# Kernel optimization log

Hardware: AMD Instinct MI355X
Metric: run time of the kernel (lower is better)

The kernel has to match this reference:

```python
import jax, jax.numpy as jnp
import numpy as np

B, D, L = 16384, 1024, 4

def setup_inputs() -> dict:
    key = jax.random.key(0)
    k1, k2 = jax.random.split(key)
    inputs = jax.random.normal(k1, (B, D), dtype=jnp.float32)
    # xavier_uniform for (D, 1): bound = sqrt(6/(D+1))
    bound = float(np.sqrt(6.0 / (D + 1)))
    weights = jax.random.uniform(k2, (L, D), dtype=jnp.float32, minval=-bound, maxval=bound)
    biases = jnp.zeros((L, D), dtype=jnp.float32)
    return {"inputs": inputs, "weights": weights, "biases": biases}

def reference(inputs, weights, biases):
    # inputs: [B, D]; weights/biases: [L, D]
    x0 = inputs

    def step(x, wb):
        w, b = wb
        xw = jnp.einsum("bd,d->b", x, w)          # x^T w  -> [B]
        x_next = x0 * xw[:, None] + b[None, :] + x  # outer product + bias + residual
        return x_next, None

    out, _ = jax.lax.scan(step, x0, (weights, biases))
    return out
```

## Files before the change

### kernel.cpp

```cpp
#include <hip/hip_runtime.h>


#define NB 16384
#define ROWS_PER_WAVE 4
#define NWAVES 4
#define ROWS_PER_BLOCK (ROWS_PER_WAVE * NWAVES)
#define NBLOCKS (NB / ROWS_PER_BLOCK)

#define DOT4(a, b) ((a).x*(b).x + (a).y*(b).y + (a).z*(b).z + (a).w*(b).w)

__global__ __launch_bounds__(256, 4) void crossnet_fused(
    const float* __restrict__ X,
    const float* __restrict__ W,
    const float* __restrict__ Bias,
    float* __restrict__ Out) {
  __shared__ float4 lds_u4[256];
  __shared__ float lds_s[NWAVES][3];

  const int t = threadIdx.x;
  const int wave = t >> 6;
  const int lane = t & 63;

  const float4* W4 = (const float4*)W;
  const float4* B4 = (const float4*)Bias;

  float4 b0 = B4[t];
  float4 b1 = B4[256 + t];
  float4 b2 = B4[512 + t];
  float4 b3 = B4[768 + t];
  float4 w1t = W4[256 + t];
  float4 w2t = W4[512 + t];
  float4 w3t = W4[768 + t];

  float4 u = b0;
  float s1p = DOT4(u, w1t);
  u.x += b1.x; u.y += b1.y; u.z += b1.z; u.w += b1.w;
  float s2p = DOT4(u, w2t);
  u.x += b2.x; u.y += b2.y; u.z += b2.z; u.w += b2.w;
  float s3p = DOT4(u, w3t);
  u.x += b3.x; u.y += b3.y; u.z += b3.z; u.w += b3.w;
  lds_u4[t] = u;

#pragma unroll
  for (int off = 32; off >= 1; off >>= 1) {
    s1p += __shfl_xor(s1p, off, 64);
    s2p += __shfl_xor(s2p, off, 64);
    s3p += __shfl_xor(s3p, off, 64);
  }
  if (lane == 0) {
    lds_s[wave][0] = s1p;
    lds_s[wave][1] = s2p;
    lds_s[wave][2] = s3p;
  }

  float4 w[4][4];
#pragma unroll
  for (int l = 0; l < 4; ++l)
#pragma unroll
    for (int k = 0; k < 4; ++k)
      w[l][k] = W4[l * 256 + lane + 64 * k];

  __syncthreads();

  const float s1 = lds_s[0][0] + lds_s[1][0] + lds_s[2][0] + lds_s[3][0];
  const float s2 = lds_s[0][1] + lds_s[1][1] + lds_s[2][1] + lds_s[3][1];
  const float s3 = lds_s[0][2] + lds_s[1][2] + lds_s[2][2] + lds_s[3][2];

  float4 u4r[4];
#pragma unroll
  for (int k = 0; k < 4; ++k) u4r[k] = lds_u4[lane + 64 * k];

  const int row0 = blockIdx.x * ROWS_PER_BLOCK + wave * ROWS_PER_WAVE;
#pragma unroll
  for (int r = 0; r < ROWS_PER_WAVE; ++r) {
    const int row = row0 + r;
    const float4* Xr = (const float4*)X + (size_t)row * 256;
    float4* Or = (float4*)Out + (size_t)row * 256;

    float4 x[4];
#pragma unroll
    for (int k = 0; k < 4; ++k) x[k] = Xr[lane + 64 * k];

    float p0 = 0.f, p1 = 0.f, p2 = 0.f, p3 = 0.f;
#pragma unroll
    for (int k = 0; k < 4; ++k) {
      p0 += DOT4(x[k], w[0][k]);
      p1 += DOT4(x[k], w[1][k]);
      p2 += DOT4(x[k], w[2][k]);
      p3 += DOT4(x[k], w[3][k]);
    }

#pragma unroll
    for (int off = 32; off >= 1; off >>= 1) {
      p0 += __shfl_xor(p0, off, 64);
      p1 += __shfl_xor(p1, off, 64);
      p2 += __shfl_xor(p2, off, 64);
      p3 += __shfl_xor(p3, off, 64);
    }

    float c = 1.0f;
    c = c * (p0 + 1.0f);
    c = c * (p1 + 1.0f) + s1;
    c = c * (p2 + 1.0f) + s2;
    c = c * (p3 + 1.0f) + s3;

#pragma unroll
    for (int k = 0; k < 4; ++k) {
      float4 o;
      o.x = c * x[k].x + u4r[k].x;
      o.y = c * x[k].y + u4r[k].y;
      o.z = c * x[k].z + u4r[k].z;
      o.w = c * x[k].w + u4r[k].w;
      Or[lane + 64 * k] = o;
    }
  }
}

extern "C" void kernel_launch(void* const* d_in, const int* in_sizes, int n_in,
                              void* d_out, int out_size, void* d_ws, size_t ws_size,
                              hipStream_t stream) {
  const float* X = (const float*)d_in[0];
  const float* W = (const float*)d_in[1];
  const float* Bias = (const float*)d_in[2];
  float* Out = (float*)d_out;

  crossnet_fused<<<NBLOCKS, 256, 0, stream>>>(X, W, Bias, Out);
}
```

Baseline: 28.80 us.

## Process one row per wave, issue X loads early, use DPP wave reductions

```diff
diff --git a/kernel.cpp b/kernel.cpp
--- a/kernel.cpp
+++ b/kernel.cpp
@@ -2,12 +2,31 @@
 
 
 #define NB 16384
-#define ROWS_PER_WAVE 4
 #define NWAVES 4
-#define ROWS_PER_BLOCK (ROWS_PER_WAVE * NWAVES)
-#define NBLOCKS (NB / ROWS_PER_BLOCK)
+#define NBLOCKS (NB / NWAVES)
 
 #define DOT4(a, b) ((a).x*(b).x + (a).y*(b).y + (a).z*(b).z + (a).w*(b).w)
+
+__device__ __forceinline__ float wave_sum64(float v) {
+  float r = v;
+  r += __int_as_float(__builtin_amdgcn_update_dpp(
+      0, __float_as_int(r), 0x111, 0xf, 0xf, false));
+  r += __int_as_float(__builtin_amdgcn_update_dpp(
+      0, __float_as_int(r), 0x112, 0xf, 0xf, false));
+  r += __int_as_float(__builtin_amdgcn_update_dpp(
+      0, __float_as_int(r), 0x114, 0xf, 0xf, false));
+  r += __int_as_float(__builtin_amdgcn_update_dpp(
+      0, __float_as_int(r), 0x118, 0xf, 0xf, false));
+  r += __int_as_float(__builtin_amdgcn_update_dpp(
+      0, __float_as_int(r), 0x142, 0xa, 0xf, false));
+  r += __int_as_float(__builtin_amdgcn_update_dpp(
+      0, __float_as_int(r), 0x143, 0xc, 0xf, false));
+  return r;
+}
+
+__device__ __forceinline__ float bcast63(float v) {
+  return __int_as_float(__builtin_amdgcn_readlane(__float_as_int(v), 63));
+}
 
 __global__ __launch_bounds__(256, 4) void crossnet_fused(
     const float* __restrict__ X,
@@ -20,9 +39,23 @@
   const int t = threadIdx.x;
   const int wave = t >> 6;
   const int lane = t & 63;
+  const int row = blockIdx.x * NWAVES + wave;
 
   const float4* W4 = (const float4*)W;
   const float4* B4 = (const float4*)Bias;
+  const float4* Xr = (const float4*)X + (size_t)row * 256;
+  float4* Or = (float4*)Out + (size_t)row * 256;
+
+  float4 x[4];
+#pragma unroll
+  for (int k = 0; k < 4; ++k) x[k] = Xr[lane + 64 * k];
+
+  float4 w[4][4];
+#pragma unroll
+  for (int l = 0; l < 4; ++l)
+#pragma unroll
+    for (int k = 0; k < 4; ++k)
+      w[l][k] = W4[l * 256 + lane + 64 * k];
 
   float4 b0 = B4[t];
   float4 b1 = B4[256 + t];
@@ -41,24 +74,27 @@
   u.x += b3.x; u.y += b3.y; u.z += b3.z; u.w += b3.w;
   lds_u4[t] = u;
 
-#pragma unroll
-  for (int off = 32; off >= 1; off >>= 1) {
-    s1p += __shfl_xor(s1p, off, 64);
-    s2p += __shfl_xor(s2p, off, 64);
-    s3p += __shfl_xor(s3p, off, 64);
-  }
-  if (lane == 0) {
+  s1p = wave_sum64(s1p);
+  s2p = wave_sum64(s2p);
+  s3p = wave_sum64(s3p);
+  if (lane == 63) {
     lds_s[wave][0] = s1p;
     lds_s[wave][1] = s2p;
     lds_s[wave][2] = s3p;
   }
 
-  float4 w[4][4];
+  float p0 = 0.f, p1 = 0.f, p2 = 0.f, p3 = 0.f;
 #pragma unroll
-  for (int l = 0; l < 4; ++l)
-#pragma unroll
-    for (int k = 0; k < 4; ++k)
-      w[l][k] = W4[l * 256 + lane + 64 * k];
+  for (int k = 0; k < 4; ++k) {
+    p0 += DOT4(x[k], w[0][k]);
+    p1 += DOT4(x[k], w[1][k]);
+    p2 += DOT4(x[k], w[2][k]);
+    p3 += DOT4(x[k], w[3][k]);
+  }
+  const float P0 = bcast63(wave_sum64(p0));
+  const float P1 = bcast63(wave_sum64(p1));
+  const float P2 = bcast63(wave_sum64(p2));
+  const float P3 = bcast63(wave_sum64(p3));
 
   __syncthreads();
 
@@ -66,53 +102,20 @@
   const float s2 = lds_s[0][1] + lds_s[1][1] + lds_s[2][1] + lds_s[3][1];
   const float s3 = lds_s[0][2] + lds_s[1][2] + lds_s[2][2] + lds_s[3][2];
 
-  float4 u4r[4];
-#pragma unroll
-  for (int k = 0; k < 4; ++k) u4r[k] = lds_u4[lane + 64 * k];
-
-  const int row0 = blockIdx.x * ROWS_PER_BLOCK + wave * ROWS_PER_WAVE;
-#pragma unroll
-  for (int r = 0; r < ROWS_PER_WAVE; ++r) {
-    const int row = row0 + r;
-    const float4* Xr = (const float4*)X + (size_t)row * 256;
-    float4* Or = (float4*)Out + (size_t)row * 256;
-
-    float4 x[4];
-#pragma unroll
-    for (int k = 0; k < 4; ++k) x[k] = Xr[lane + 64 * k];
-
-    float p0 = 0.f, p1 = 0.f, p2 = 0.f, p3 = 0.f;
-#pragma unroll
-    for (int k = 0; k < 4; ++k) {
-      p0 += DOT4(x[k], w[0][k]);
-      p1 += DOT4(x[k], w[1][k]);
-      p2 += DOT4(x[k], w[2][k]);
-      p3 += DOT4(x[k], w[3][k]);
-    }
+  float c = P0 + 1.0f;
+  c = c * (P1 + 1.0f) + s1;
+  c = c * (P2 + 1.0f) + s2;
+  c = c * (P3 + 1.0f) + s3;
 
 #pragma unroll
-    for (int off = 32; off >= 1; off >>= 1) {
-      p0 += __shfl_xor(p0, off, 64);
-      p1 += __shfl_xor(p1, off, 64);
-      p2 += __shfl_xor(p2, off, 64);
-      p3 += __shfl_xor(p3, off, 64);
-    }
-
-    float c = 1.0f;
-    c = c * (p0 + 1.0f);
-    c = c * (p1 + 1.0f) + s1;
-    c = c * (p2 + 1.0f) + s2;
-    c = c * (p3 + 1.0f) + s3;
-
-#pragma unroll
-    for (int k = 0; k < 4; ++k) {
-      float4 o;
-      o.x = c * x[k].x + u4r[k].x;
-      o.y = c * x[k].y + u4r[k].y;
-      o.z = c * x[k].z + u4r[k].z;
-      o.w = c * x[k].w + u4r[k].w;
-      Or[lane + 64 * k] = o;
-    }
+  for (int k = 0; k < 4; ++k) {
+    float4 u4r = lds_u4[lane + 64 * k];
+    float4 o;
+    o.x = c * x[k].x + u4r.x;
+    o.y = c * x[k].y + u4r.y;
+    o.z = c * x[k].z + u4r.z;
+    o.w = c * x[k].w + u4r.w;
+    Or[lane + 64 * k] = o;
   }
 }
 
```

Result: faster. 26.91 us (-6.6%).
